# Kernel tuning notes

Hardware: AMD Instinct MI355X
Metric: run time of the kernel (lower is better)

Reference implementation:

```python
import jax, jax.numpy as jnp
import numpy as np

N_HEAD = 16
HEAD = 64
EMBED = 1024
TOP_K_RATIO = 0.1
MASKED = True
B, T = 2, 2048


def setup_inputs() -> dict:
    key = jax.random.key(0)
    ks = jax.random.split(key, 7)
    w = lambda k, shape: jax.random.normal(k, shape, jnp.float32) * 0.02
    return {
        "index": jax.random.normal(ks[0], (B, T, EMBED), jnp.float32),
        "memory": jax.random.normal(ks[1], (B, T, EMBED), jnp.float32),
        "Wq": w(ks[2], (N_HEAD, EMBED, HEAD)),
        "Wk": w(ks[3], (N_HEAD, EMBED, HEAD)),
        "Wv": w(ks[4], (N_HEAD, EMBED, HEAD)),
        "W_proj": w(ks[5], (N_HEAD * HEAD, EMBED)),
        "b_proj": jnp.zeros((EMBED,), jnp.float32),
    }


def reference(index, memory, Wq, Wk, Wv, W_proj, b_proj):
    b, t, e = index.shape
    s = memory.shape[1]
    # All heads batched: [B, H, T, D]
    q = jnp.einsum("bte,hed->bhtd", index, Wq)
    k = jnp.einsum("bse,hed->bhsd", memory, Wk)
    v = jnp.einsum("bse,hed->bhsd", memory, Wv)
    scores = jnp.einsum("bhtd,bhsd->bhts", q, k) * (HEAD ** -0.5)  # [B,H,T,S]
    neg_inf = jnp.array(-jnp.inf, scores.dtype)
    if MASKED:
        causal = jnp.tril(jnp.ones((t, s), bool))
        scores = jnp.where(causal, scores, neg_inf)
    # top-k sparsification: keep only the top ceil(ratio*S) scores per query row
    k_top = max(1, int(TOP_K_RATIO * s))
    thresh = jax.lax.top_k(scores, k_top)[0][..., -1:]  # kth largest per row
    scores = jnp.where(scores >= thresh, scores, neg_inf)
    att = jax.nn.softmax(scores, axis=-1)
    out = jnp.einsum("bhts,bhsd->bhtd", att, v)
    # concat heads along feature dim: [B, T, H*D]
    out = out.transpose(0, 2, 1, 3).reshape(b, t, N_HEAD * HEAD)
    return out @ W_proj + b_proj  # dropout is identity at eval
```

## Files before the change

### kernel.cpp

```cpp
#include <hip/hip_runtime.h>
#include <hip/hip_bf16.h>

#define TT 2048
#define KTOP 204
#define ROWS 16
#define SCS 2056
#define HSTR 130

typedef float f32x4 __attribute__((ext_vector_type(4)));
typedef short short8 __attribute__((ext_vector_type(8)));
typedef unsigned short u16;
typedef unsigned int u32;
typedef u32 u32x2 __attribute__((ext_vector_type(2)));
typedef u32 u32x4 __attribute__((ext_vector_type(4)));

static __device__ __forceinline__ f32x4 mfma16(short8 a, short8 b, f32x4 c) {
  return __builtin_amdgcn_mfma_f32_16x16x32_bf16(a, b, c, 0, 0, 0);
}

static __device__ __forceinline__ u16 f2b(float f) {
  __hip_bfloat16 h = __float2bfloat16(f);
  return *reinterpret_cast<u16*>(&h);
}

static __device__ __forceinline__ u32 cvt_pk_bf16(float lo, float hi) {
  u32 r;
  asm("v_cvt_pk_bf16_f32 %0, %1, %2" : "=v"(r) : "v"(lo), "v"(hi));
  return r;
}

#define GLOAD16(gp, lp) __builtin_amdgcn_global_load_lds( \
    (const __attribute__((address_space(1))) void*)(gp),  \
    (__attribute__((address_space(3))) void*)(lp), 16, 0, 0)

#define WSYNC() do { __builtin_amdgcn_wave_barrier(); \
    asm volatile("s_waitcnt lgkmcnt(0)" ::: "memory"); \
    __builtin_amdgcn_wave_barrier(); } while (0)

static __device__ __forceinline__ void radix_rank(int h0, int h1c, int h2c,
                                                  int h3c, int lane, int& k,
                                                  u32& digOut) {
  int lsum = h0 + h1c + h2c + h3c;
  int ssum = lsum;
#pragma unroll
  for (int off = 1; off < 64; off <<= 1) {
    int o = __shfl_down(ssum, off);
    ssum += (lane + off < 64) ? o : 0;
  }
  int above = ssum - lsum;
  int cg3 = above;
  int cg2 = cg3 + h3c;
  int cg1 = cg2 + h2c;
  int cg0 = cg1 + h1c;
  int idx = lane * 4;
  int dig = -1, nk = 0;
  if (cg0 < k && cg0 + h0 >= k) { dig = idx;     nk = k - cg0; }
  if (cg1 < k && cg1 + h1c >= k) { dig = idx + 1; nk = k - cg1; }
  if (cg2 < k && cg2 + h2c >= k) { dig = idx + 2; nk = k - cg2; }
  if (cg3 < k && cg3 + h3c >= k) { dig = idx + 3; nk = k - cg3; }
  unsigned long long ball = __ballot(dig >= 0);
  int src = __ffsll((long long)ball) - 1;
  dig = __shfl(dig, src);
  nk = __shfl(nk, src);
  digOut = (u32)dig;
  k = nk;
}

template <int JMAX>
static __device__ __forceinline__ void select_softmax(
    u16* __restrict__ sc, const u32* __restrict__ hist8,
    u32* __restrict__ h2w, float* __restrict__ rs, int w, int lane, int t0) {
  const int NI = JMAX * 4;
  int row0 = w, row1 = w + 8;
  bool sel0 = t0 + row0 + 1 > KTOP, sel1 = t0 + row1 + 1 > KTOP;

  u32 rv0[NI], rv1[NI];
#pragma unroll
  for (int j = 0; j < JMAX; ++j) {
    u32x4 v0 = *(const u32x4*)&sc[row0 * SCS + lane * 8 + j * 512];
    u32x4 v1 = *(const u32x4*)&sc[row1 * SCS + lane * 8 + j * 512];
    rv0[j*4+0] = v0[0]; rv0[j*4+1] = v0[1]; rv0[j*4+2] = v0[2]; rv0[j*4+3] = v0[3];
    rv1[j*4+0] = v1[0]; rv1[j*4+1] = v1[1]; rv1[j*4+2] = v1[2]; rv1[j*4+3] = v1[3];
  }

  u32 a0w = hist8[row0 * HSTR + lane * 2], a1w = hist8[row0 * HSTR + lane * 2 + 1];
  u32 b0w = hist8[row1 * HSTR + lane * 2], b1w = hist8[row1 * HSTR + lane * 2 + 1];

  int lt0 = lane * 4 + ((a1w >> 16) ? 3 : ((a1w & 0xFFFFu) ? 2
                       : ((a0w >> 16) ? 1 : 0)));
  int lt1 = lane * 4 + ((b1w >> 16) ? 3 : ((b1w & 0xFFFFu) ? 2
                       : ((b0w >> 16) ? 1 : 0)));
  unsigned long long bl0 = __ballot((a0w | a1w) != 0);
  unsigned long long bl1 = __ballot((b0w | b1w) != 0);
  int top0 = __shfl(lt0, 63 - __builtin_clzll(bl0));
  int top1 = __shfl(lt1, 63 - __builtin_clzll(bl1));
  u32 ref0 = ((u32)top0 << 8) + 255u;
  u32 ref1 = ((u32)top1 << 8) + 255u;

  u32 keyth0 = 0, keyth1 = 0;
  int k0 = KTOP, k1 = KTOP;
  u32 d1_0 = 0, d1_1 = 0, d;
  if (sel0) {
    radix_rank((int)(a0w & 0xFFFF), (int)(a0w >> 16),
               (int)(a1w & 0xFFFF), (int)(a1w >> 16), lane, k0, d1_0);
  }
  if (sel1) {
    radix_rank((int)(b0w & 0xFFFF), (int)(b0w >> 16),
               (int)(b1w & 0xFFFF), (int)(b1w >> 16), lane, k1, d1_1);
  }

  if (sel0) {
    h2w[lane] = 0; h2w[lane + 64] = 0;
    WSYNC();
#pragma unroll
    for (int i = 0; i < NI; ++i) {
      u32 p = rv0[i];
      u32 e0 = p & 0xFFFFu, e1 = p >> 16;
      if ((e0 >> 8) == d1_0)
        atomicAdd(&h2w[(e0 & 255u) >> 1], 1u << ((e0 & 1u) << 4));
      if ((e1 >> 8) == d1_0)
        atomicAdd(&h2w[(e1 & 255u) >> 1], 1u << ((e1 & 1u) << 4));
    }
    WSYNC();
    u32 w0 = h2w[lane * 2], w1 = h2w[lane * 2 + 1];
    radix_rank((int)(w0 & 0xFFFF), (int)(w0 >> 16),
               (int)(w1 & 0xFFFF), (int)(w1 >> 16), lane, k0, d);
    keyth0 = (d1_0 << 8) | d;
  }
  if (sel1) {
    h2w[lane] = 0; h2w[lane + 64] = 0;
    WSYNC();
#pragma unroll
    for (int i = 0; i < NI; ++i) {
      u32 p = rv1[i];
      u32 e0 = p & 0xFFFFu, e1 = p >> 16;
      if ((e0 >> 8) == d1_1)
        atomicAdd(&h2w[(e0 & 255u) >> 1], 1u << ((e0 & 1u) << 4));
      if ((e1 >> 8) == d1_1)
        atomicAdd(&h2w[(e1 & 255u) >> 1], 1u << ((e1 & 1u) << 4));
    }
    WSYNC();
    u32 w0 = h2w[lane * 2], w1 = h2w[lane * 2 + 1];
    radix_rank((int)(w0 & 0xFFFF), (int)(w0 >> 16),
               (int)(w1 & 0xFFFF), (int)(w1 >> 16), lane, k1, d);
    keyth1 = (d1_1 << 8) | d;
  }

  u32 thr0 = keyth0 > 1u ? keyth0 : 1u;
  u32 thr1 = keyth1 > 1u ? keyth1 : 1u;
  const float c2 = 1.44269504f / 4096.f;
  float sum0 = 0.f, sum1 = 0.f;
#pragma unroll
  for (int i = 0; i < NI; ++i) {
    u32 p0 = rv0[i], p1 = rv1[i];
    u32 a0 = p0 & 0xFFFFu, a1 = p0 >> 16;
    u32 b0 = p1 & 0xFFFFu, b1 = p1 >> 16;
    float pa0 = (a0 >= thr0) ? exp2f((float)(int)(a0 - ref0) * c2) : 0.f;
    float pa1 = (a1 >= thr0) ? exp2f((float)(int)(a1 - ref0) * c2) : 0.f;
    float pb0 = (b0 >= thr1) ? exp2f((float)(int)(b0 - ref1) * c2) : 0.f;
    float pb1 = (b1 >= thr1) ? exp2f((float)(int)(b1 - ref1) * c2) : 0.f;
    sum0 += pa0 + pa1;
    sum1 += pb0 + pb1;
    rv0[i] = cvt_pk_bf16(pa0, pa1);
    rv1[i] = cvt_pk_bf16(pb0, pb1);
  }
#pragma unroll
  for (int off = 32; off; off >>= 1) {
    sum0 += __shfl_xor(sum0, off);
    sum1 += __shfl_xor(sum1, off);
  }
#pragma unroll
  for (int j = 0; j < JMAX; ++j) {
    *(u32x4*)&sc[row0 * SCS + lane * 8 + j * 512] =
        (u32x4){rv0[j*4+0], rv0[j*4+1], rv0[j*4+2], rv0[j*4+3]};
    *(u32x4*)&sc[row1 * SCS + lane * 8 + j * 512] =
        (u32x4){rv1[j*4+0], rv1[j*4+1], rv1[j*4+2], rv1[j*4+3]};
  }
  if (lane == 0) {
    rs[row0] = 1.f / fmaxf(sum0, 1e-30f);
    rs[row1] = 1.f / fmaxf(sum1, 1e-30f);
  }
}


__global__ __launch_bounds__(256) void k_cast2(const float* __restrict__ in0,
                                               const float* __restrict__ in1,
                                               u16* __restrict__ o0,
                                               u16* __restrict__ o1) {
  const float* in = blockIdx.z ? in1 : in0;
  u16* out = blockIdx.z ? o1 : o0;
  int i = (blockIdx.x * 256 + threadIdx.x) * 4;
  f32x4 v = *(const f32x4*)(in + i);
  u16 r0 = f2b(v[0]), r1 = f2b(v[1]), r2 = f2b(v[2]), r3 = f2b(v[3]);
  out[i] = r0; out[i+1] = r1; out[i+2] = r2; out[i+3] = r3;
}

__global__ __launch_bounds__(256) void k_tw3(
    const float* __restrict__ W0, const float* __restrict__ W1,
    const float* __restrict__ W2, u16* __restrict__ o0,
    u16* __restrict__ o1, u16* __restrict__ o2) {
  int z = blockIdx.z;
  const float* W = z == 0 ? W0 : (z == 1 ? W1 : W2);
  u16* out = z == 0 ? o0 : (z == 1 ? o1 : o2);
  int i = blockIdx.x * 256 + threadIdx.x;
  int d = i & 63, e = (i >> 6) & 1023, h = i >> 16;
  out[(h * 64 + d) * 1024 + e] = f2b(W[i]);
}

__global__ __launch_bounds__(256) void k_tsq(const float* __restrict__ W,
                                             u16* __restrict__ out) {
  int i = blockIdx.x * 256 + threadIdx.x;
  int n = i & 1023, kk = i >> 10;
  out[n * 1024 + kk] = f2b(W[i]);
}

static __device__ __forceinline__ void gemm_core(
    const u16* __restrict__ A, const u16* __restrict__ Bt, int m0, int n0,
    int tid, u16 (*lA)[2048], u16 (*lB)[2048], f32x4* acc) {
  const int K = 1024;
  int w = tid >> 6, lane = tid & 63;
  int lr = lane & 15, lg = lane >> 4;
  const u16* ga = A + (size_t)(m0 + (tid >> 2)) * K + (tid & 3) * 8;
  const u16* gb = Bt + (size_t)(n0 + (tid >> 2)) * K + (tid & 3) * 8;
  char* a0 = (char*)lA[0] + w * 1024;
  char* a1 = (char*)lA[1] + w * 1024;
  char* b0 = (char*)lB[0] + w * 1024;
  char* b1 = (char*)lB[1] + w * 1024;

  for (int kt = 0; kt < K; kt += 64) {
    __syncthreads();
    GLOAD16(ga + kt, a0);
    GLOAD16(gb + kt, b0);
    GLOAD16(ga + kt + 32, a1);
    GLOAD16(gb + kt + 32, b1);
    __syncthreads();
#pragma unroll
    for (int p = 0; p < 2; ++p) {
      short8 a = *(const short8*)&lA[p][(w * 16 + lr) * 32 + lg * 8];
#pragma unroll
      for (int j = 0; j < 4; ++j) {
        short8 b = *(const short8*)&lB[p][(j * 16 + lr) * 32 + lg * 8];
        acc[j] = mfma16(a, b, acc[j]);
      }
    }
  }
}

__global__ __launch_bounds__(256) void gemm_qkv(
    const u16* __restrict__ xbi, const u16* __restrict__ xbm,
    const u16* __restrict__ wqt, const u16* __restrict__ wkt,
    const u16* __restrict__ wvt, u16* __restrict__ qb,
    u16* __restrict__ kbf, u16* __restrict__ vtb) {
  __shared__ u16 lA[2][2048], lB[2][2048];
  int tid = threadIdx.x, z = blockIdx.z;
  int m0 = blockIdx.y * 64, n0 = blockIdx.x * 64;
  const u16* A = z ? xbm : xbi;
  const u16* Bt = z == 0 ? wqt : (z == 1 ? wkt : wvt);
  f32x4 acc[4] = {};
  gemm_core(A, Bt, m0, n0, tid, lA, lB, acc);

  int w = tid >> 6, lane = tid & 63, lr = lane & 15, lg = lane >> 4;
  float ascale = (z == 0) ? 0.125f : 1.f;
  u16* out0 = (z == 0) ? qb : kbf;
  int mbase = m0 + w * 16 + lg * 4;
#pragma unroll
  for (int j = 0; j < 4; ++j) {
    int n = n0 + j * 16 + lr;
#pragma unroll
    for (int jj = 0; jj < 4; ++jj) {
      int m = mbase + jj;
      float v = acc[j][jj];
      int b = m >> 11, t = m & 2047, h = n >> 6, dd = n & 63;
      if (z == 2)
        vtb[(((size_t)(b * 16 + h)) * 64 + dd) * TT + t] = f2b(v);
      else
        out0[(((size_t)(b * 16 + h)) * TT + t) * 64 + dd] = f2b(v * ascale);
    }
  }
}

__global__ __launch_bounds__(256) void gemm_proj(
    const u16* __restrict__ A, const u16* __restrict__ Bt,
    float* __restrict__ outp, const float* __restrict__ bias) {
  __shared__ u16 lA[2][2048], lB[2][2048];
  int tid = threadIdx.x;
  int m0 = blockIdx.y * 64, n0 = blockIdx.x * 64;
  f32x4 acc[4] = {};
  gemm_core(A, Bt, m0, n0, tid, lA, lB, acc);

  int w = tid >> 6, lane = tid & 63, lr = lane & 15, lg = lane >> 4;
  int mbase = m0 + w * 16 + lg * 4;
#pragma unroll
  for (int j = 0; j < 4; ++j) {
    int n = n0 + j * 16 + lr;
#pragma unroll
    for (int jj = 0; jj < 4; ++jj) {
      int m = mbase + jj;
      outp[(size_t)m * 1024 + n] = acc[j][jj] + bias[n];
    }
  }
}

__global__ __launch_bounds__(512, 4) void k_attn(
    const u16* __restrict__ qb, const u16* __restrict__ kb,
    const u16* __restrict__ vtb, u16* __restrict__ aob) {
  __shared__ u16 sc[ROWS * SCS];
  __shared__ u32 aux[3104];
  __shared__ float rs[ROWS];

  u32* hist8 = aux;
  u32* h2 = aux + 2080;

  int tid = threadIdx.x, w = tid >> 6, lane = tid & 63;
  int lr = lane & 15, lg = lane >> 4;
  int bid = blockIdx.x + 128 * blockIdx.y;
  int swz = (bid & 7) * 512 + (bid >> 3);
  int t0 = (swz & 127) * ROWS;
  int bh = swz >> 7;
  const u16* qh = qb + (size_t)bh * TT * 64;
  const u16* kh = kb + (size_t)bh * TT * 64;
  const u16* vh = vtb + (size_t)bh * 64 * TT;
  int SC = ((t0 + ROWS + 31) >> 5) << 5;
  int jmax = (SC + 511) >> 9;

  for (int i = tid; i < ROWS * HSTR; i += 512) hist8[i] = 0;

  short8 qf0 = *(const short8*)&qh[(size_t)(t0 + lr) * 64 + lg * 8];
  short8 qf1 = *(const short8*)&qh[(size_t)(t0 + lr) * 64 + 32 + lg * 8];
  __syncthreads();

  {
    int t = t0 + lr;
    int s0 = w * 16;
    short8 kc0, kc1, kn0, kn1;
    if (s0 < SC) {
      kc0 = *(const short8*)&kh[(size_t)(s0 + lr) * 64 + lg * 8];
      kc1 = *(const short8*)&kh[(size_t)(s0 + lr) * 64 + 32 + lg * 8];
      if (s0 + 128 < SC) {
        kn0 = *(const short8*)&kh[(size_t)(s0 + 128 + lr) * 64 + lg * 8];
        kn1 = *(const short8*)&kh[(size_t)(s0 + 128 + lr) * 64 + 32 + lg * 8];
      }
    }
    for (; s0 < SC; s0 += 128) {
      f32x4 acc = {0.f, 0.f, 0.f, 0.f};
      acc = mfma16(kc0, qf0, acc);
      acc = mfma16(kc1, qf1, acc);
      kc0 = kn0; kc1 = kn1;
      if (s0 + 256 < SC) {
        kn0 = *(const short8*)&kh[(size_t)(s0 + 256 + lr) * 64 + lg * 8];
        kn1 = *(const short8*)&kh[(size_t)(s0 + 256 + lr) * 64 + 32 + lg * 8];
      }
      int sbase = s0 + lg * 4;
      u32 key[4];
      if (s0 + 15 <= t0) {
#pragma unroll
        for (int j = 0; j < 4; ++j) {
          float kf = fmaf(acc[j], 4096.f, 32768.f);
          key[j] = (u32)fminf(fmaxf(kf, 0.f), 65535.f);
        }
      } else {
#pragma unroll
        for (int j = 0; j < 4; ++j) {
          float kf = fmaf(acc[j], 4096.f, 32768.f);
          key[j] = (u32)fminf(fmaxf(kf, 0.f), 65535.f);
          if (sbase + j > t) key[j] = 0;
        }
      }
#pragma unroll
      for (int j = 0; j < 4; ++j)
        atomicAdd(&hist8[lr * HSTR + (key[j] >> 9)],
                  1u << (((key[j] >> 8) & 1u) << 4));
      *(u32x2*)&sc[lr * SCS + sbase] =
          (u32x2){key[0] | (key[1] << 16), key[2] | (key[3] << 16)};
    }
  }
  {
    int fillEnd = jmax << 9;
    for (int r = 0; r < ROWS; ++r)
      for (int s = SC + tid * 8; s < fillEnd; s += 512 * 8)
        *(u32x4*)&sc[r * SCS + s] = (u32x4){0, 0, 0, 0};
  }
  __syncthreads();

  switch (jmax) {
    case 1: select_softmax<1>(sc, hist8, &h2[w * 128], rs, w, lane, t0); break;
    case 2: select_softmax<2>(sc, hist8, &h2[w * 128], rs, w, lane, t0); break;
    case 3: select_softmax<3>(sc, hist8, &h2[w * 128], rs, w, lane, t0); break;
    default: select_softmax<4>(sc, hist8, &h2[w * 128], rs, w, lane, t0); break;
  }
  __syncthreads();

  float* po = (float*)aux;
  int d0 = (w & 3) * 16;
  int h = w >> 2;
  int tiles = SC >> 5;
  int mid = ((tiles + 1) >> 1) << 5;
  int kb0 = h ? mid : 0;
  int kb1 = h ? SC : mid;
  f32x4 o = {0.f, 0.f, 0.f, 0.f};
  {
    int kk = kb0;
    short8 bn;
    if (kk < kb1)
      bn = *(const short8*)&vh[(size_t)(d0 + lr) * TT + kk + lg * 8];
    for (; kk < kb1; kk += 32) {
      short8 b = bn;
      int kn = kk + 32;
      if (kn < kb1)
        bn = *(const short8*)&vh[(size_t)(d0 + lr) * TT + kn + lg * 8];
      short8 a = *(const short8*)&sc[lr * SCS + kk + lg * 8];
      o = mfma16(a, b, o);
    }
  }
#pragma unroll
  for (int j = 0; j < 4; ++j)
    po[(h * ROWS + lg * 4 + j) * 68 + d0 + lr] = o[j];
  __syncthreads();

  if (w < 4) {
    int b_ = bh >> 4, h_ = bh & 15;
    int dd0 = w * 16;
#pragma unroll
    for (int j = 0; j < 4; ++j) {
      int row = lg * 4 + j;
      float val = (po[row * 68 + dd0 + lr] + po[(ROWS + row) * 68 + dd0 + lr]) *
                  rs[row];
      aob[((size_t)(b_ * TT + t0 + row)) * 1024 + h_ * 64 + dd0 + lr] = f2b(val);
    }
  }
}


extern "C" void kernel_launch(void* const* d_in, const int* in_sizes, int n_in,
                              void* d_out, int out_size, void* d_ws, size_t ws_size,
                              hipStream_t stream) {
  const float* index  = (const float*)d_in[0];
  const float* memory = (const float*)d_in[1];
  const float* Wq     = (const float*)d_in[2];
  const float* Wk     = (const float*)d_in[3];
  const float* Wv     = (const float*)d_in[4];
  const float* Wp     = (const float*)d_in[5];
  const float* bp     = (const float*)d_in[6];

  char* ws = (char*)d_ws;
  const size_t MB = 1024 * 1024;
  u16* xbi = (u16*)(ws + 0);
  u16* xbm = (u16*)(ws + 8 * MB);
  u16* wqt = (u16*)(ws + 16 * MB);
  u16* wkt = (u16*)(ws + 18 * MB);
  u16* wvt = (u16*)(ws + 20 * MB);
  u16* wpt = (u16*)(ws + 22 * MB);
  u16* qb  = (u16*)(ws + 24 * MB);
  u16* kbf = (u16*)(ws + 32 * MB);
  u16* vtb = (u16*)(ws + 40 * MB);
  u16* aob = xbi;

  k_cast2<<<dim3(4096, 1, 2), 256, 0, stream>>>(index, memory, xbi, xbm);
  k_tw3<<<dim3(4096, 1, 3), 256, 0, stream>>>(Wq, Wk, Wv, wqt, wkt, wvt);
  k_tsq<<<4096, 256, 0, stream>>>(Wp, wpt);

  gemm_qkv<<<dim3(16, 64, 3), 256, 0, stream>>>(xbi, xbm, wqt, wkt, wvt,
                                                qb, kbf, vtb);

  k_attn<<<dim3(128, 32), 512, 0, stream>>>(qb, kbf, vtb, aob);

  gemm_proj<<<dim3(16, 64), 256, 0, stream>>>(aob, wpt, (float*)d_out, bp);
}
```

Measured before the change: 281.8 us.

## Merge prep kernels and enlarge GEMM tiles to 128x64 with packed V stores

The three cast/transpose prep kernels are merged into one launch with six z-slices, which saves launch overhead. Both GEMMs now use a 128x64 tile: each wave computes two 16-row M sub-tiles and reuses its B fragments across them, halving the grid in M and cutting B reloads per output. The V-transpose epilogue packs four bf16 values into one 8-byte store instead of four scalar stores. In exchange each block uses more LDS and registers, and there are fewer blocks, which may lower occupancy.

Measured after the change: 262.7 us. 1.07x faster.

```diff
diff --git a/kernel.cpp b/kernel.cpp
--- a/kernel.cpp
+++ b/kernel.cpp
@@ -182,45 +182,40 @@
   }
 }
 
-
-__global__ __launch_bounds__(256) void k_cast2(const float* __restrict__ in0,
-                                               const float* __restrict__ in1,
-                                               u16* __restrict__ o0,
-                                               u16* __restrict__ o1) {
-  const float* in = blockIdx.z ? in1 : in0;
-  u16* out = blockIdx.z ? o1 : o0;
-  int i = (blockIdx.x * 256 + threadIdx.x) * 4;
-  f32x4 v = *(const f32x4*)(in + i);
-  u16 r0 = f2b(v[0]), r1 = f2b(v[1]), r2 = f2b(v[2]), r3 = f2b(v[3]);
-  out[i] = r0; out[i+1] = r1; out[i+2] = r2; out[i+3] = r3;
-}
-
-__global__ __launch_bounds__(256) void k_tw3(
-    const float* __restrict__ W0, const float* __restrict__ W1,
-    const float* __restrict__ W2, u16* __restrict__ o0,
-    u16* __restrict__ o1, u16* __restrict__ o2) {
+__global__ __launch_bounds__(256) void k_prep(
+    const float* __restrict__ index, const float* __restrict__ memory,
+    const float* __restrict__ Wq, const float* __restrict__ Wk,
+    const float* __restrict__ Wv, const float* __restrict__ Wp,
+    u16* __restrict__ xbi, u16* __restrict__ xbm, u16* __restrict__ wqt,
+    u16* __restrict__ wkt, u16* __restrict__ wvt, u16* __restrict__ wpt) {
   int z = blockIdx.z;
-  const float* W = z == 0 ? W0 : (z == 1 ? W1 : W2);
-  u16* out = z == 0 ? o0 : (z == 1 ? o1 : o2);
   int i = blockIdx.x * 256 + threadIdx.x;
-  int d = i & 63, e = (i >> 6) & 1023, h = i >> 16;
-  out[(h * 64 + d) * 1024 + e] = f2b(W[i]);
-}
-
-__global__ __launch_bounds__(256) void k_tsq(const float* __restrict__ W,
-                                             u16* __restrict__ out) {
-  int i = blockIdx.x * 256 + threadIdx.x;
-  int n = i & 1023, kk = i >> 10;
-  out[n * 1024 + kk] = f2b(W[i]);
-}
-
-static __device__ __forceinline__ void gemm_core(
+  if (z < 2) {
+    const float* in = z ? memory : index;
+    u16* out = z ? xbm : xbi;
+    int i4 = i * 4;
+    f32x4 v = *(const f32x4*)(in + i4);
+    u16 r0 = f2b(v[0]), r1 = f2b(v[1]), r2 = f2b(v[2]), r3 = f2b(v[3]);
+    out[i4] = r0; out[i4+1] = r1; out[i4+2] = r2; out[i4+3] = r3;
+  } else if (z < 5) {
+    const float* W = z == 2 ? Wq : (z == 3 ? Wk : Wv);
+    u16* out = z == 2 ? wqt : (z == 3 ? wkt : wvt);
+    int d = i & 63, e = (i >> 6) & 1023, h = i >> 16;
+    out[(h * 64 + d) * 1024 + e] = f2b(W[i]);
+  } else {
+    int n = i & 1023, kk = i >> 10;
+    wpt[n * 1024 + kk] = f2b(Wp[i]);
+  }
+}
+
+static __device__ __forceinline__ void gemm_core128(
     const u16* __restrict__ A, const u16* __restrict__ Bt, int m0, int n0,
-    int tid, u16 (*lA)[2048], u16 (*lB)[2048], f32x4* acc) {
+    int tid, u16 (*lA)[4096], u16 (*lB)[2048], f32x4 (*acc)[4]) {
   const int K = 1024;
   int w = tid >> 6, lane = tid & 63;
   int lr = lane & 15, lg = lane >> 4;
-  const u16* ga = A + (size_t)(m0 + (tid >> 2)) * K + (tid & 3) * 8;
+  const u16* ga0 = A + (size_t)(m0 + (tid >> 2)) * K + (tid & 3) * 8;
+  const u16* ga1 = A + (size_t)(m0 + 64 + (tid >> 2)) * K + (tid & 3) * 8;
   const u16* gb = Bt + (size_t)(n0 + (tid >> 2)) * K + (tid & 3) * 8;
   char* a0 = (char*)lA[0] + w * 1024;
   char* a1 = (char*)lA[1] + w * 1024;
@@ -229,19 +224,27 @@
 
   for (int kt = 0; kt < K; kt += 64) {
     __syncthreads();
-    GLOAD16(ga + kt, a0);
+    GLOAD16(ga0 + kt, a0);
+    GLOAD16(ga1 + kt, a0 + 4096);
     GLOAD16(gb + kt, b0);
-    GLOAD16(ga + kt + 32, a1);
+    GLOAD16(ga0 + kt + 32, a1);
+    GLOAD16(ga1 + kt + 32, a1 + 4096);
     GLOAD16(gb + kt + 32, b1);
     __syncthreads();
 #pragma unroll
     for (int p = 0; p < 2; ++p) {
-      short8 a = *(const short8*)&lA[p][(w * 16 + lr) * 32 + lg * 8];
-#pragma unroll
-      for (int j = 0; j < 4; ++j) {
-        short8 b = *(const short8*)&lB[p][(j * 16 + lr) * 32 + lg * 8];
-        acc[j] = mfma16(a, b, acc[j]);
-      }
+      short8 af[2], bf[4];
+#pragma unroll
+      for (int mq = 0; mq < 2; ++mq)
+        af[mq] = *(const short8*)&lA[p][(w * 32 + mq * 16 + lr) * 32 + lg * 8];
+#pragma unroll
+      for (int nq = 0; nq < 4; ++nq)
+        bf[nq] = *(const short8*)&lB[p][(nq * 16 + lr) * 32 + lg * 8];
+#pragma unroll
+      for (int mq = 0; mq < 2; ++mq)
+#pragma unroll
+        for (int nq = 0; nq < 4; ++nq)
+          acc[mq][nq] = mfma16(af[mq], bf[nq], acc[mq][nq]);
     }
   }
 }
@@ -251,30 +254,39 @@
     const u16* __restrict__ wqt, const u16* __restrict__ wkt,
     const u16* __restrict__ wvt, u16* __restrict__ qb,
     u16* __restrict__ kbf, u16* __restrict__ vtb) {
-  __shared__ u16 lA[2][2048], lB[2][2048];
+  __shared__ u16 lA[2][4096], lB[2][2048];
   int tid = threadIdx.x, z = blockIdx.z;
-  int m0 = blockIdx.y * 64, n0 = blockIdx.x * 64;
+  int m0 = blockIdx.y * 128, n0 = blockIdx.x * 64;
   const u16* A = z ? xbm : xbi;
   const u16* Bt = z == 0 ? wqt : (z == 1 ? wkt : wvt);
-  f32x4 acc[4] = {};
-  gemm_core(A, Bt, m0, n0, tid, lA, lB, acc);
+  f32x4 acc[2][4] = {};
+  gemm_core128(A, Bt, m0, n0, tid, lA, lB, acc);
 
   int w = tid >> 6, lane = tid & 63, lr = lane & 15, lg = lane >> 4;
   float ascale = (z == 0) ? 0.125f : 1.f;
   u16* out0 = (z == 0) ? qb : kbf;
-  int mbase = m0 + w * 16 + lg * 4;
-#pragma unroll
-  for (int j = 0; j < 4; ++j) {
-    int n = n0 + j * 16 + lr;
-#pragma unroll
-    for (int jj = 0; jj < 4; ++jj) {
-      int m = mbase + jj;
-      float v = acc[j][jj];
-      int b = m >> 11, t = m & 2047, h = n >> 6, dd = n & 63;
-      if (z == 2)
-        vtb[(((size_t)(b * 16 + h)) * 64 + dd) * TT + t] = f2b(v);
-      else
-        out0[(((size_t)(b * 16 + h)) * TT + t) * 64 + dd] = f2b(v * ascale);
+#pragma unroll
+  for (int mq = 0; mq < 2; ++mq) {
+    int mbase = m0 + w * 32 + mq * 16 + lg * 4;
+    int b = mbase >> 11;
+#pragma unroll
+    for (int nq = 0; nq < 4; ++nq) {
+      int n = n0 + nq * 16 + lr;
+      int h = n >> 6, dd = n & 63;
+      if (z == 2) {
+        u32 lo = cvt_pk_bf16(acc[mq][nq][0], acc[mq][nq][1]);
+        u32 hi = cvt_pk_bf16(acc[mq][nq][2], acc[mq][nq][3]);
+        *(u32x2*)&vtb[(((size_t)(b * 16 + h)) * 64 + dd) * TT + (mbase & 2047)] =
+            (u32x2){lo, hi};
+      } else {
+#pragma unroll
+        for (int jj = 0; jj < 4; ++jj) {
+          int m = mbase + jj;
+          int t = m & 2047;
+          out0[(((size_t)(b * 16 + h)) * TT + t) * 64 + dd] =
+              f2b(acc[mq][nq][jj] * ascale);
+        }
+      }
     }
   }
 }
@@ -282,21 +294,23 @@
 __global__ __launch_bounds__(256) void gemm_proj(
     const u16* __restrict__ A, const u16* __restrict__ Bt,
     float* __restrict__ outp, const float* __restrict__ bias) {
-  __shared__ u16 lA[2][2048], lB[2][2048];
+  __shared__ u16 lA[2][4096], lB[2][2048];
   int tid = threadIdx.x;
-  int m0 = blockIdx.y * 64, n0 = blockIdx.x * 64;
-  f32x4 acc[4] = {};
-  gemm_core(A, Bt, m0, n0, tid, lA, lB, acc);
+  int m0 = blockIdx.y * 128, n0 = blockIdx.x * 64;
+  f32x4 acc[2][4] = {};
+  gemm_core128(A, Bt, m0, n0, tid, lA, lB, acc);
 
   int w = tid >> 6, lane = tid & 63, lr = lane & 15, lg = lane >> 4;
-  int mbase = m0 + w * 16 + lg * 4;
-#pragma unroll
-  for (int j = 0; j < 4; ++j) {
-    int n = n0 + j * 16 + lr;
-#pragma unroll
-    for (int jj = 0; jj < 4; ++jj) {
-      int m = mbase + jj;
-      outp[(size_t)m * 1024 + n] = acc[j][jj] + bias[n];
+#pragma unroll
+  for (int mq = 0; mq < 2; ++mq) {
+    int mbase = m0 + w * 32 + mq * 16 + lg * 4;
+#pragma unroll
+    for (int nq = 0; nq < 4; ++nq) {
+      int n = n0 + nq * 16 + lr;
+      float bi = bias[n];
+#pragma unroll
+      for (int jj = 0; jj < 4; ++jj)
+        outp[(size_t)(mbase + jj) * 1024 + n] = acc[mq][nq][jj] + bi;
     }
   }
 }
@@ -455,14 +469,13 @@
   u16* vtb = (u16*)(ws + 40 * MB);
   u16* aob = xbi;
 
-  k_cast2<<<dim3(4096, 1, 2), 256, 0, stream>>>(index, memory, xbi, xbm);
-  k_tw3<<<dim3(4096, 1, 3), 256, 0, stream>>>(Wq, Wk, Wv, wqt, wkt, wvt);
-  k_tsq<<<4096, 256, 0, stream>>>(Wp, wpt);
-
-  gemm_qkv<<<dim3(16, 64, 3), 256, 0, stream>>>(xbi, xbm, wqt, wkt, wvt,
+  k_prep<<<dim3(4096, 1, 6), 256, 0, stream>>>(index, memory, Wq, Wk, Wv, Wp,
+                                               xbi, xbm, wqt, wkt, wvt, wpt);
+
+  gemm_qkv<<<dim3(16, 32, 3), 256, 0, stream>>>(xbi, xbm, wqt, wkt, wvt,
                                                 qb, kbf, vtb);
 
   k_attn<<<dim3(128, 32), 512, 0, stream>>>(qb, kbf, vtb, aob);
 
-  gemm_proj<<<dim3(16, 64), 256, 0, stream>>>(aob, wpt, (float*)d_out, bp);
-}
+  gemm_proj<<<dim3(16, 32), 256, 0, stream>>>(aob, wpt, (float*)d_out, bp);
+}
```
